# Optimization experiments

Measured on AMD Instinct MI355X. Metric: run time of the kernel, lower is better.

The kernel has to match this reference:

```python
import jax, jax.numpy as jnp
import numpy as np

N = 50000      # nodes
E = 800000     # edges (avg degree 16)
F_IN = 128     # num_node_features
H = 128        # hidden_channels
B = 64         # graphs in batch
OUT = 1        # output_features


def setup_inputs() -> dict:
    key = jax.random.key(0)
    ks = jax.random.split(key, 12)
    def lin_w(k, fan_in, fan_out):
        return (jax.random.normal(k, (fan_in, fan_out), jnp.float32)
                / np.float32(np.sqrt(fan_in)))
    x = jax.random.normal(ks[0], (N, F_IN), jnp.float32)
    edge_index = jax.random.randint(ks[1], (2, E), 0, N, dtype=jnp.int32)
    batch = jnp.sort(jax.random.randint(ks[2], (N,), 0, B, dtype=jnp.int32))
    return dict(
        x=x, edge_index=edge_index, batch=batch,
        W1=lin_w(ks[3], F_IN, H), b1=jnp.zeros((H,), jnp.float32),
        W2=lin_w(ks[4], H, H),    b2=jnp.zeros((H,), jnp.float32),
        W3=lin_w(ks[5], H, H),    b3=jnp.zeros((H,), jnp.float32),
        fw1=lin_w(ks[6], H, 64),  fb1=jnp.zeros((64,), jnp.float32),
        fw2=lin_w(ks[7], 64, OUT), fb2=jnp.zeros((OUT,), jnp.float32),
    )


def _gcn_conv(x, W, b, src, dst, norm, n_nodes):
    # h = X W; out[i] = sum_{j->i} norm_ij * h[j] + b  (self-loops included in src/dst)
    h = x @ W
    msg = h[src] * norm[:, None]                       # [E+N, H] gather + scale
    return jax.ops.segment_sum(msg, dst, num_segments=n_nodes) + b


def reference(x, edge_index, batch, W1, b1, W2, b2, W3, b3, fw1, fb1, fw2, fb2):
    src, dst = edge_index[0], edge_index[1]
    loop = jnp.arange(N, dtype=src.dtype)
    src = jnp.concatenate([src, loop])                 # add self-loops
    dst = jnp.concatenate([dst, loop])
    deg = jax.ops.segment_sum(jnp.ones_like(dst, jnp.float32), dst,
                              num_segments=N)
    dinv = jax.lax.rsqrt(jnp.maximum(deg, 1.0))        # deg^{-1/2}
    norm = dinv[src] * dinv[dst]                       # symmetric GCN norm per edge

    h = jax.nn.relu(_gcn_conv(x, W1, b1, src, dst, norm, N))
    h = jax.nn.relu(_gcn_conv(h, W2, b2, src, dst, norm, N))
    h = _gcn_conv(h, W3, b3, src, dst, norm, N)

    # global mean pool over graph ids
    sums = jax.ops.segment_sum(h, batch, num_segments=B)
    cnt = jax.ops.segment_sum(jnp.ones((N,), jnp.float32), batch,
                              num_segments=B)
    g = sums / jnp.maximum(cnt, 1.0)[:, None]          # [B, H]

    g = jax.nn.relu(g @ fw1 + fb1)
    return g @ fw2 + fb2                               # [B, OUT]
```

## Files before the change

### kernel.cpp

```cpp
#include <hip/hip_runtime.h>
#include <math.h>

#define N_NODES 50000
#define N_PAD   50048
#define N_EDGES 800000
#define F 128
#define FH 64
#define B_GRAPHS 64
#define SCAN_NB 49
#define N_INT4 12500

using bf16x8 = __attribute__((ext_vector_type(8))) short;
using f32x4  = __attribute__((ext_vector_type(4))) float;
union U4 { uint4 u; bf16x8 v; };


__device__ __forceinline__ unsigned bf16_rne(float a) {
    unsigned u = __float_as_uint(a);
    u += 0x7fffu + ((u >> 16) & 1u);
    return u >> 16;
}

__device__ __forceinline__ unsigned pack_bf16x2(float a, float b) {
    return bf16_rne(a) | (bf16_rne(b) << 16);
}

__device__ __forceinline__ float2 unpack_bf16x2(unsigned p) {
    return make_float2(__uint_as_float(p << 16),
                       __uint_as_float(p & 0xffff0000u));
}

__device__ __forceinline__ void split2(float a, float b, unsigned& hiw, unsigned& low) {
    unsigned ha = bf16_rne(a), hb = bf16_rne(b);
    float ra = a - __uint_as_float(ha << 16);
    float rb = b - __uint_as_float(hb << 16);
    hiw = ha | (hb << 16);
    low = pack_bf16x2(ra, rb);
}


__global__ __launch_bounds__(256) void zero_i32(int* p, int n) {
    int i = blockIdx.x * blockDim.x + threadIdx.x;
    if (i < n) p[i] = 0;
}

__global__ __launch_bounds__(256) void zero_f32(float* p, int n) {
    int i = blockIdx.x * blockDim.x + threadIdx.x;
    if (i < n) p[i] = 0.f;
}


__global__ __launch_bounds__(256) void deg_count(const int* __restrict__ dst,
                                                 int* __restrict__ deg) {
    int e = blockIdx.x * blockDim.x + threadIdx.x;
    if (e < N_EDGES) atomicAdd(&deg[dst[e]], 1);
}

__global__ __launch_bounds__(256) void dinv_kernel(const int* __restrict__ deg,
                                                   float* __restrict__ dinv) {
    int i = blockIdx.x * blockDim.x + threadIdx.x;
    if (i < N_NODES) dinv[i] = rsqrtf((float)(deg[i] + 1));
}


__global__ __launch_bounds__(256) void scan1(const int* __restrict__ deg,
                                             int* __restrict__ off,
                                             int* __restrict__ bsum) {
    __shared__ int wsum[4];
    int b = blockIdx.x, t = threadIdx.x;
    int i4 = b * 256 + t;
    int4 v = make_int4(0, 0, 0, 0);
    if (i4 < N_INT4) v = ((const int4*)deg)[i4];
    int s = v.x + v.y + v.z + v.w;
    int lane = t & 63;
    int incl = s;
#pragma unroll
    for (int d = 1; d < 64; d <<= 1) {
        int u = __shfl_up(incl, d, 64);
        if (lane >= d) incl += u;
    }
    int wave = t >> 6;
    if (lane == 63) wsum[wave] = incl;
    __syncthreads();
    int woff = 0;
#pragma unroll
    for (int w = 0; w < 3; ++w) if (w < wave) woff += wsum[w];
    int texcl = woff + incl - s;
    int4 o;
    o.x = texcl;
    o.y = o.x + v.x;
    o.z = o.y + v.y;
    o.w = o.z + v.z;
    if (i4 < N_INT4) ((int4*)off)[i4] = o;
    if (t == 255) bsum[b] = woff + incl;
}

__global__ __launch_bounds__(64) void scan2(const int* __restrict__ bsum,
                                            int* __restrict__ bexcl,
                                            int* __restrict__ off) {
    int t = threadIdx.x;
    int v = (t < SCAN_NB) ? bsum[t] : 0;
    int incl = v;
#pragma unroll
    for (int d = 1; d < 64; d <<= 1) {
        int u = __shfl_up(incl, d, 64);
        if (t >= d) incl += u;
    }
    if (t < SCAN_NB) bexcl[t] = incl - v;
    if (t == 63) off[N_NODES] = incl;
}

__global__ __launch_bounds__(256) void scan3(int* __restrict__ off,
                                             int* __restrict__ cursor,
                                             const int* __restrict__ bexcl) {
    int b = blockIdx.x, t = threadIdx.x;
    int i4 = b * 256 + t;
    if (i4 >= N_INT4) return;
    int add = bexcl[b];
    int4 o = ((int4*)off)[i4];
    o.x += add; o.y += add; o.z += add; o.w += add;
    ((int4*)off)[i4] = o;
    ((int4*)cursor)[i4] = o;
}

__global__ __launch_bounds__(256) void scatter_kernel(const int* __restrict__ src,
                                                      const int* __restrict__ dst,
                                                      int* __restrict__ cursor,
                                                      int* __restrict__ srcs) {
    int e = blockIdx.x * blockDim.x + threadIdx.x;
    if (e < N_EDGES) {
        int d = dst[e];
        int p = atomicAdd(&cursor[d], 1);
        srcs[p] = src[e];
    }
}


__global__ __launch_bounds__(256) void conv_x(const float* __restrict__ x,
                                              unsigned* __restrict__ Xhi,
                                              unsigned* __restrict__ Xlo) {
    int gid = blockIdx.x * 256 + threadIdx.x;
    if (gid >= N_NODES * FH) return;
    float2 v = *(const float2*)&x[(size_t)gid * 2];
    unsigned hw, lw;
    split2(v.x, v.y, hw, lw);
    Xhi[gid] = hw;
    Xlo[gid] = lw;
}

__global__ __launch_bounds__(256) void conv_w(const float* __restrict__ W,
                                              unsigned* __restrict__ Wfh,
                                              unsigned* __restrict__ Wfl) {
    int pos = blockIdx.x * 256 + threadIdx.x;
    if (pos >= 2048) return;
    int lane = pos & 63;
    int kc = (pos >> 6) & 3;
    int nt = pos >> 8;
    int col = nt * 16 + (lane & 15);
    int kg = lane >> 4;
    uint4 hw, lw;
    unsigned* hp = (unsigned*)&hw;
    unsigned* lp = (unsigned*)&lw;
#pragma unroll
    for (int w = 0; w < 4; ++w) {
        int k0 = kc * 32 + kg * 8 + 2 * w;
        float a = W[(size_t)k0 * F + col];
        float b = W[(size_t)(k0 + 1) * F + col];
        split2(a, b, hp[w], lp[w]);
    }
    ((uint4*)Wfh)[pos] = hw;
    ((uint4*)Wfl)[pos] = lw;
}


__global__ __launch_bounds__(256) void gemm_mfma(const unsigned* __restrict__ Xhi,
                                                 const unsigned* __restrict__ Xlo,
                                                 const unsigned* __restrict__ Wfh,
                                                 const unsigned* __restrict__ Wfl,
                                                 const float* __restrict__ dinv,
                                                 unsigned* __restrict__ Hs) {
    __shared__ uint4 lxh[64 * 16];
    __shared__ uint4 lxl[64 * 16];
    const int tid = threadIdx.x;
    const int m0 = blockIdx.x * 64;

#pragma unroll
    for (int i = 0; i < 4; ++i) {
        int idx = i * 256 + tid;
        int row = idx >> 4;
        int g = idx & 15;
        int gs = g ^ (row & 7);
        lxh[row * 16 + gs] = ((const uint4*)Xhi)[(size_t)(m0 + row) * 16 + g];
        lxl[row * 16 + gs] = ((const uint4*)Xlo)[(size_t)(m0 + row) * 16 + g];
    }
    __syncthreads();

    const int wave = tid >> 6, lane = tid & 63;
    const int lr = lane & 15, kg = lane >> 4;
    const int r = wave * 16 + lr;

    f32x4 acc[8];
#pragma unroll
    for (int nt = 0; nt < 8; ++nt) acc[nt] = (f32x4){0.f, 0.f, 0.f, 0.f};

#pragma unroll
    for (int kc = 0; kc < 4; ++kc) {
        int gs = (kc * 4 + kg) ^ (r & 7);
        U4 ah, al;
        ah.u = lxh[r * 16 + gs];
        al.u = lxl[r * 16 + gs];
#pragma unroll
        for (int nt = 0; nt < 8; ++nt) {
            U4 bh, bl;
            bh.u = ((const uint4*)Wfh)[(nt * 4 + kc) * 64 + lane];
            bl.u = ((const uint4*)Wfl)[(nt * 4 + kc) * 64 + lane];
            acc[nt] = __builtin_amdgcn_mfma_f32_16x16x32_bf16(ah.v, bh.v, acc[nt], 0, 0, 0);
            acc[nt] = __builtin_amdgcn_mfma_f32_16x16x32_bf16(ah.v, bl.v, acc[nt], 0, 0, 0);
            acc[nt] = __builtin_amdgcn_mfma_f32_16x16x32_bf16(al.v, bh.v, acc[nt], 0, 0, 0);
        }
    }

#pragma unroll
    for (int rr = 0; rr < 4; ++rr) {
        int row = m0 + wave * 16 + 4 * kg + rr;
        bool ok = row < N_NODES;
        float s = ok ? dinv[row] : 0.f;
#pragma unroll
        for (int nt = 0; nt < 8; ++nt) {
            float v = acc[nt][rr] * s;
            float pv = __shfl_xor(v, 1, 64);
            if (((lane & 1) == 0) && ok) {
                Hs[(size_t)row * FH + ((nt * 16 + lr) >> 1)] = pack_bf16x2(v, pv);
            }
        }
    }
}


__device__ __forceinline__ float2 edge_sum(const unsigned* __restrict__ Hs,
                                           const int* __restrict__ off,
                                           const int* __restrict__ srcs,
                                           int node, int lane) {
    float2 acc = unpack_bf16x2(Hs[(size_t)node * FH + lane]);
    int e0 = off[node], e1 = off[node + 1];
    int e = e0;
    for (; e + 7 < e1; e += 8) {
        int si[8];
#pragma unroll
        for (int j = 0; j < 8; ++j) si[j] = srcs[e + j];
        unsigned p[8];
#pragma unroll
        for (int j = 0; j < 8; ++j) p[j] = Hs[(size_t)si[j] * FH + lane];
        float2 t0 = unpack_bf16x2(p[0]), t1 = unpack_bf16x2(p[1]);
        float2 t2 = unpack_bf16x2(p[2]), t3 = unpack_bf16x2(p[3]);
        float2 t4 = unpack_bf16x2(p[4]), t5 = unpack_bf16x2(p[5]);
        float2 t6 = unpack_bf16x2(p[6]), t7 = unpack_bf16x2(p[7]);
        acc.x += ((t0.x + t1.x) + (t2.x + t3.x)) + ((t4.x + t5.x) + (t6.x + t7.x));
        acc.y += ((t0.y + t1.y) + (t2.y + t3.y)) + ((t4.y + t5.y) + (t6.y + t7.y));
    }
    for (; e < e1; ++e) {
        float2 v = unpack_bf16x2(Hs[(size_t)srcs[e] * FH + lane]);
        acc.x += v.x;
        acc.y += v.y;
    }
    return acc;
}


__global__ __launch_bounds__(256) void aggregate_bf16(const unsigned* __restrict__ Hs,
                                                      const int* __restrict__ off,
                                                      const int* __restrict__ srcs,
                                                      const float* __restrict__ dinv,
                                                      const float* __restrict__ bias,
                                                      unsigned* __restrict__ Xhi,
                                                      unsigned* __restrict__ Xlo) {
    int node = blockIdx.x * 4 + (threadIdx.x >> 6);
    if (node >= N_NODES) return;
    int lane = threadIdx.x & 63;
    float2 acc = edge_sum(Hs, off, srcs, node, lane);
    float d = dinv[node];
    float o0 = fmaxf(fmaf(d, acc.x, bias[2 * lane]), 0.f);
    float o1 = fmaxf(fmaf(d, acc.y, bias[2 * lane + 1]), 0.f);
    unsigned hw, lw;
    split2(o0, o1, hw, lw);
    Xhi[(size_t)node * FH + lane] = hw;
    Xlo[(size_t)node * FH + lane] = lw;
}


__global__ __launch_bounds__(256) void aggregate_pool(const unsigned* __restrict__ Hs,
                                                      const int* __restrict__ off,
                                                      const int* __restrict__ srcs,
                                                      const float* __restrict__ dinv,
                                                      const float* __restrict__ bias,
                                                      const int* __restrict__ batch,
                                                      float* __restrict__ psums) {
    int wg = (blockIdx.x * 256 + threadIdx.x) >> 6;
    int lane = threadIdx.x & 63;
    int n0 = wg * 8;
    if (n0 >= N_NODES) return;
    int n1 = n0 + 8;
    if (n1 > N_NODES) n1 = N_NODES;

    float bx = bias[2 * lane], by = bias[2 * lane + 1];
    float2 racc = make_float2(0.f, 0.f);
    int cur = batch[n0];
    for (int node = n0; node < n1; ++node) {
        float2 acc = edge_sum(Hs, off, srcs, node, lane);
        float d = dinv[node];
        float o0 = fmaf(d, acc.x, bx);
        float o1 = fmaf(d, acc.y, by);
        int b = batch[node];
        if (b != cur) {
            atomicAdd(&psums[cur * F + 2 * lane], racc.x);
            atomicAdd(&psums[cur * F + 2 * lane + 1], racc.y);
            racc = make_float2(0.f, 0.f);
            cur = b;
        }
        racc.x += o0;
        racc.y += o1;
    }
    atomicAdd(&psums[cur * F + 2 * lane], racc.x);
    atomicAdd(&psums[cur * F + 2 * lane + 1], racc.y);
}


__device__ __forceinline__ int lower_bound_dev(const int* __restrict__ a, int n, int v) {
    int lo = 0, hi = n;
    while (lo < hi) {
        int m = (lo + hi) >> 1;
        if (a[m] < v) lo = m + 1; else hi = m;
    }
    return lo;
}

__global__ __launch_bounds__(128) void pool_finalize(const float* __restrict__ psums,
                                                     const int* __restrict__ batch,
                                                     float* __restrict__ g) {
    int b = blockIdx.x;
    int f = threadIdx.x;
    int lo = lower_bound_dev(batch, N_NODES, b);
    int hi = lower_bound_dev(batch, N_NODES, b + 1);
    float cnt = (float)(hi - lo);
    g[b * F + f] = psums[b * F + f] / fmaxf(cnt, 1.0f);
}


__global__ __launch_bounds__(64) void head_kernel(const float* __restrict__ g,
                                                  const float* __restrict__ fw1,
                                                  const float* __restrict__ fb1,
                                                  const float* __restrict__ fw2,
                                                  const float* __restrict__ fb2,
                                                  float* __restrict__ out) {
    int b = blockIdx.x;
    int j = threadIdx.x;
    float h = fb1[j];
    for (int k = 0; k < F; ++k)
        h = fmaf(g[b * F + k], fw1[k * 64 + j], h);
    h = fmaxf(h, 0.f) * fw2[j];
#pragma unroll
    for (int w = 32; w >= 1; w >>= 1) h += __shfl_xor(h, w, 64);
    if (j == 0) out[b] = h + fb2[0];
}


extern "C" void kernel_launch(void* const* d_in, const int* in_sizes, int n_in,
                              void* d_out, int out_size, void* d_ws, size_t ws_size,
                              hipStream_t stream) {
    const float* x    = (const float*)d_in[0];
    const int* eidx   = (const int*)d_in[1];
    const int* batch  = (const int*)d_in[2];
    const float* W1   = (const float*)d_in[3];
    const float* b1   = (const float*)d_in[4];
    const float* W2   = (const float*)d_in[5];
    const float* b2   = (const float*)d_in[6];
    const float* W3   = (const float*)d_in[7];
    const float* b3   = (const float*)d_in[8];
    const float* fw1  = (const float*)d_in[9];
    const float* fb1  = (const float*)d_in[10];
    const float* fw2  = (const float*)d_in[11];
    const float* fb2  = (const float*)d_in[12];
    float* out        = (float*)d_out;

    const int* src = eidx;
    const int* dst = eidx + N_EDGES;

    char* ws = (char*)d_ws;
    size_t p = 0;
    auto alloc = [&](size_t bytes) -> void* {
        void* r = ws + p;
        p = (p + bytes + 255) & ~(size_t)255;
        return r;
    };
    int*      deg    = (int*)     alloc((size_t)N_NODES * 4);
    float*    dinv   = (float*)   alloc((size_t)N_NODES * 4);
    int*      off    = (int*)     alloc((size_t)(N_NODES + 4) * 4);
    int*      cursor = (int*)     alloc((size_t)N_NODES * 4);
    int*      srcs   = (int*)     alloc((size_t)N_EDGES * 4);
    int*      bsum   = (int*)     alloc((size_t)SCAN_NB * 4);
    int*      bexcl  = (int*)     alloc((size_t)SCAN_NB * 4);
    unsigned* XpkHi  = (unsigned*)alloc((size_t)N_PAD * FH * 4);
    unsigned* XpkLo  = (unsigned*)alloc((size_t)N_PAD * FH * 4);
    unsigned* HsPk   = (unsigned*)alloc((size_t)N_PAD * FH * 4);
    unsigned* Wf     = (unsigned*)alloc((size_t)6 * 2048 * 16);
    float*    psums  = (float*)   alloc((size_t)B_GRAPHS * F * 4);
    float*    gpool  = (float*)   alloc((size_t)B_GRAPHS * F * 4);
    (void)ws_size;

    unsigned* Wf1h = Wf + 0 * 8192;
    unsigned* Wf1l = Wf + 1 * 8192;
    unsigned* Wf2h = Wf + 2 * 8192;
    unsigned* Wf2l = Wf + 3 * 8192;
    unsigned* Wf3h = Wf + 4 * 8192;
    unsigned* Wf3l = Wf + 5 * 8192;

    const int TB = 256;
    const int nblk_N = (N_NODES + TB - 1) / TB;
    const int nblk_E = (N_EDGES + TB - 1) / TB;
    const int gemm_blocks = N_PAD / 64;
    const int agg_blocks = (N_NODES + 3) / 4;
    const int aggp_blocks = (6250 + 3) / 4 + 1;
    const int convx_blocks = (N_NODES * FH + TB - 1) / TB;

    zero_i32<<<nblk_N, TB, 0, stream>>>(deg, N_NODES);
    deg_count<<<nblk_E, TB, 0, stream>>>(dst, deg);
    dinv_kernel<<<nblk_N, TB, 0, stream>>>(deg, dinv);

    scan1<<<SCAN_NB, 256, 0, stream>>>(deg, off, bsum);
    scan2<<<1, 64, 0, stream>>>(bsum, bexcl, off);
    scan3<<<SCAN_NB, 256, 0, stream>>>(off, cursor, bexcl);
    scatter_kernel<<<nblk_E, TB, 0, stream>>>(src, dst, cursor, srcs);

    conv_x<<<convx_blocks, TB, 0, stream>>>(x, XpkHi, XpkLo);
    conv_w<<<8, TB, 0, stream>>>(W1, Wf1h, Wf1l);
    conv_w<<<8, TB, 0, stream>>>(W2, Wf2h, Wf2l);
    conv_w<<<8, TB, 0, stream>>>(W3, Wf3h, Wf3l);
    zero_f32<<<(B_GRAPHS * F + TB - 1) / TB, TB, 0, stream>>>(psums, B_GRAPHS * F);

    gemm_mfma<<<gemm_blocks, 256, 0, stream>>>(XpkHi, XpkLo, Wf1h, Wf1l, dinv, HsPk);
    aggregate_bf16<<<agg_blocks, 256, 0, stream>>>(HsPk, off, srcs, dinv, b1, XpkHi, XpkLo);

    gemm_mfma<<<gemm_blocks, 256, 0, stream>>>(XpkHi, XpkLo, Wf2h, Wf2l, dinv, HsPk);
    aggregate_bf16<<<agg_blocks, 256, 0, stream>>>(HsPk, off, srcs, dinv, b2, XpkHi, XpkLo);

    gemm_mfma<<<gemm_blocks, 256, 0, stream>>>(XpkHi, XpkLo, Wf3h, Wf3l, dinv, HsPk);
    aggregate_pool<<<aggp_blocks, 256, 0, stream>>>(HsPk, off, srcs, dinv, b3, batch, psums);

    pool_finalize<<<B_GRAPHS, 128, 0, stream>>>(psums, batch, gpool);
    head_kernel<<<B_GRAPHS, 64, 0, stream>>>(gpool, fw1, fb1, fw2, fb2, out);
}
```

Before: 391.8 us.

## Replace atomic CSR scatter with two-pass bucketed scatter and widen edge gather unroll

```diff
diff --git a/kernel.cpp b/kernel.cpp
--- a/kernel.cpp
+++ b/kernel.cpp
@@ -9,6 +9,8 @@
 #define B_GRAPHS 64
 #define SCAN_NB 49
 #define N_INT4 12500
+#define NBUCKET 196
+#define SCAT_CHUNK 4096
 
 using bf16x8 = __attribute__((ext_vector_type(8))) short;
 using f32x4  = __attribute__((ext_vector_type(4))) float;
@@ -111,7 +113,6 @@
 }
 
 __global__ __launch_bounds__(256) void scan3(int* __restrict__ off,
-                                             int* __restrict__ cursor,
                                              const int* __restrict__ bexcl) {
     int b = blockIdx.x, t = threadIdx.x;
     int i4 = b * 256 + t;
@@ -120,18 +121,64 @@
     int4 o = ((int4*)off)[i4];
     o.x += add; o.y += add; o.z += add; o.w += add;
     ((int4*)off)[i4] = o;
-    ((int4*)cursor)[i4] = o;
-}
-
-__global__ __launch_bounds__(256) void scatter_kernel(const int* __restrict__ src,
+}
+
+
+__global__ __launch_bounds__(256) void init_bcursor(const int* __restrict__ off,
+                                                    int* __restrict__ bcursor) {
+    int t = threadIdx.x;
+    if (t < NBUCKET) bcursor[t] = off[t << 8];
+}
+
+__global__ __launch_bounds__(256) void scatter_bucket(const int* __restrict__ src,
                                                       const int* __restrict__ dst,
-                                                      int* __restrict__ cursor,
-                                                      int* __restrict__ srcs) {
-    int e = blockIdx.x * blockDim.x + threadIdx.x;
-    if (e < N_EDGES) {
-        int d = dst[e];
-        int p = atomicAdd(&cursor[d], 1);
-        srcs[p] = src[e];
+                                                      int* __restrict__ bcursor,
+                                                      unsigned* __restrict__ pairs) {
+    __shared__ int lcnt[NBUCKET];
+    __shared__ int lbase[NBUCKET];
+    int t = threadIdx.x;
+    int base = blockIdx.x * SCAT_CHUNK;
+    for (int i = t; i < NBUCKET; i += 256) lcnt[i] = 0;
+    __syncthreads();
+#pragma unroll
+    for (int i = 0; i < SCAT_CHUNK / 256; ++i) {
+        int idx = base + i * 256 + t;
+        if (idx < N_EDGES) atomicAdd(&lcnt[dst[idx] >> 8], 1);
+    }
+    __syncthreads();
+    for (int i = t; i < NBUCKET; i += 256) {
+        lbase[i] = atomicAdd(&bcursor[i], lcnt[i]);
+        lcnt[i] = 0;
+    }
+    __syncthreads();
+#pragma unroll
+    for (int i = 0; i < SCAT_CHUNK / 256; ++i) {
+        int idx = base + i * 256 + t;
+        if (idx < N_EDGES) {
+            int s = src[idx], d = dst[idx];
+            int b = d >> 8;
+            int pos = lbase[b] + atomicAdd(&lcnt[b], 1);
+            pairs[pos] = (unsigned)s | ((unsigned)(d & 255) << 17);
+        }
+    }
+}
+
+__global__ __launch_bounds__(256) void scatter_place(const unsigned* __restrict__ pairs,
+                                                     const int* __restrict__ off,
+                                                     int* __restrict__ srcs) {
+    __shared__ int lcur[256];
+    int b = blockIdx.x;
+    int n0 = b << 8;
+    int t = threadIdx.x;
+    int nodeEnd = n0 + 256; if (nodeEnd > N_NODES) nodeEnd = N_NODES;
+    if (n0 + t < N_NODES) lcur[t] = off[n0 + t];
+    int start = off[n0];
+    int end = off[nodeEnd];
+    __syncthreads();
+    for (int p = start + t; p < end; p += 256) {
+        unsigned pr = pairs[p];
+        int pos = atomicAdd(&lcur[pr >> 17], 1);
+        srcs[pos] = (int)(pr & 0x1FFFFu);
     }
 }
 
@@ -244,19 +291,34 @@
     float2 acc = unpack_bf16x2(Hs[(size_t)node * FH + lane]);
     int e0 = off[node], e1 = off[node + 1];
     int e = e0;
-    for (; e + 7 < e1; e += 8) {
-        int si[8];
-#pragma unroll
-        for (int j = 0; j < 8; ++j) si[j] = srcs[e + j];
-        unsigned p[8];
-#pragma unroll
-        for (int j = 0; j < 8; ++j) p[j] = Hs[(size_t)si[j] * FH + lane];
+    for (; e + 15 < e1; e += 16) {
+        int si[16];
+#pragma unroll
+        for (int j = 0; j < 16; ++j) si[j] = srcs[e + j];
+        unsigned p[16];
+#pragma unroll
+        for (int j = 0; j < 16; ++j) p[j] = Hs[(size_t)si[j] * FH + lane];
+        float sx = 0.f, sy = 0.f;
+#pragma unroll
+        for (int j = 0; j < 16; ++j) {
+            float2 v = unpack_bf16x2(p[j]);
+            sx += v.x;
+            sy += v.y;
+        }
+        acc.x += sx;
+        acc.y += sy;
+    }
+    for (; e + 3 < e1; e += 4) {
+        int si[4];
+#pragma unroll
+        for (int j = 0; j < 4; ++j) si[j] = srcs[e + j];
+        unsigned p[4];
+#pragma unroll
+        for (int j = 0; j < 4; ++j) p[j] = Hs[(size_t)si[j] * FH + lane];
         float2 t0 = unpack_bf16x2(p[0]), t1 = unpack_bf16x2(p[1]);
         float2 t2 = unpack_bf16x2(p[2]), t3 = unpack_bf16x2(p[3]);
-        float2 t4 = unpack_bf16x2(p[4]), t5 = unpack_bf16x2(p[5]);
-        float2 t6 = unpack_bf16x2(p[6]), t7 = unpack_bf16x2(p[7]);
-        acc.x += ((t0.x + t1.x) + (t2.x + t3.x)) + ((t4.x + t5.x) + (t6.x + t7.x));
-        acc.y += ((t0.y + t1.y) + (t2.y + t3.y)) + ((t4.y + t5.y) + (t6.y + t7.y));
+        acc.x += (t0.x + t1.x) + (t2.x + t3.x);
+        acc.y += (t0.y + t1.y) + (t2.y + t3.y);
     }
     for (; e < e1; ++e) {
         float2 v = unpack_bf16x2(Hs[(size_t)srcs[e] * FH + lane]);
@@ -395,10 +457,10 @@
     int*      deg    = (int*)     alloc((size_t)N_NODES * 4);
     float*    dinv   = (float*)   alloc((size_t)N_NODES * 4);
     int*      off    = (int*)     alloc((size_t)(N_NODES + 4) * 4);
-    int*      cursor = (int*)     alloc((size_t)N_NODES * 4);
     int*      srcs   = (int*)     alloc((size_t)N_EDGES * 4);
     int*      bsum   = (int*)     alloc((size_t)SCAN_NB * 4);
     int*      bexcl  = (int*)     alloc((size_t)SCAN_NB * 4);
+    int*      bcursor= (int*)     alloc((size_t)NBUCKET * 4);
     unsigned* XpkHi  = (unsigned*)alloc((size_t)N_PAD * FH * 4);
     unsigned* XpkLo  = (unsigned*)alloc((size_t)N_PAD * FH * 4);
     unsigned* HsPk   = (unsigned*)alloc((size_t)N_PAD * FH * 4);
@@ -407,6 +469,8 @@
     float*    gpool  = (float*)   alloc((size_t)B_GRAPHS * F * 4);
     (void)ws_size;
 
+    unsigned* pairs = HsPk;
+
     unsigned* Wf1h = Wf + 0 * 8192;
     unsigned* Wf1l = Wf + 1 * 8192;
     unsigned* Wf2h = Wf + 2 * 8192;
@@ -421,6 +485,7 @@
     const int agg_blocks = (N_NODES + 3) / 4;
     const int aggp_blocks = (6250 + 3) / 4 + 1;
     const int convx_blocks = (N_NODES * FH + TB - 1) / TB;
+    const int scatA_blocks = (N_EDGES + SCAT_CHUNK - 1) / SCAT_CHUNK;
 
     zero_i32<<<nblk_N, TB, 0, stream>>>(deg, N_NODES);
     deg_count<<<nblk_E, TB, 0, stream>>>(dst, deg);
@@ -428,8 +493,10 @@
 
     scan1<<<SCAN_NB, 256, 0, stream>>>(deg, off, bsum);
     scan2<<<1, 64, 0, stream>>>(bsum, bexcl, off);
-    scan3<<<SCAN_NB, 256, 0, stream>>>(off, cursor, bexcl);
-    scatter_kernel<<<nblk_E, TB, 0, stream>>>(src, dst, cursor, srcs);
+    scan3<<<SCAN_NB, 256, 0, stream>>>(off, bexcl);
+    init_bcursor<<<1, 256, 0, stream>>>(off, bcursor);
+    scatter_bucket<<<scatA_blocks, 256, 0, stream>>>(src, dst, bcursor, pairs);
+    scatter_place<<<NBUCKET, 256, 0, stream>>>(pairs, off, srcs);
 
     conv_x<<<convx_blocks, TB, 0, stream>>>(x, XpkHi, XpkLo);
     conv_w<<<8, TB, 0, stream>>>(W1, Wf1h, Wf1l);
```

After: 348.2 us. -11.1%, faster.
